# Performance work log

Measured on AMD Instinct MI355X. Metric: run time of the kernel, lower is better.

## Reference

```python
import jax, jax.numpy as jnp
import numpy as np

M, K, N = 32, 8192, 8192      # tokens, infeatures, outfeatures
GROUP = 128                   # quantization group size along K
PACK = 8                      # 32 bits / 4 bits per value


def _dequant(qweight, scales):
    """Unpack int4 nibbles (packed 8-per-int32 along K) and apply per-group
    symmetric dequant: w = (q - 8) * scale, matching Marlin's fused dequant."""
    kp, n = qweight.shape  # (K//8, N)
    shifts = (4 * jnp.arange(PACK, dtype=jnp.int32))[None, :, None]
    q = ((qweight[:, None, :] >> shifts) & 15)          # (K//8, 8, N)
    q = q.reshape(kp * PACK, n).astype(jnp.float32)     # (K, N)
    groups = scales.shape[0]
    gsz = (kp * PACK) // groups
    w = (q.reshape(groups, gsz, n) - 8.0) * scales[:, None, :]
    return w.reshape(kp * PACK, n)                      # (K, N) fp


def setup_inputs() -> dict:
    key = jax.random.key(0)
    kA, kQ, kS, kB = jax.random.split(key, 4)
    A = jax.random.normal(kA, (M, K), jnp.float32)
    # draw raw 4-bit codes then pack 8 of them into each int32 along K
    q4 = jax.random.randint(kQ, (K, N), 0, 16, jnp.int32)
    shifts = (4 * jnp.arange(PACK, dtype=jnp.int32))[None, :, None]
    qweight = jnp.sum(q4.reshape(K // PACK, PACK, N) << shifts, axis=1).astype(jnp.int32)
    scales = jax.random.uniform(kS, (K // GROUP, N), jnp.float32, 0.005, 0.02)
    bias = jax.random.normal(kB, (N,), jnp.float32) * 0.01
    return {"A": A, "qweight": qweight, "scales": scales, "bias": bias}


def reference(A, qweight, scales, bias):
    # Marlin mul(A, B, C, s) computes C = A @ dequant(B, s); then + bias
    W = _dequant(qweight, scales)          # (K, N)
    return A @ W + bias                    # (M, N)
```

## Files before the change

### kernel.cpp

```cpp
#include <hip/hip_runtime.h>
#include <hip/hip_bf16.h>
#include <stdint.h>

#define M_DIM 32
#define K_DIM 8192
#define N_DIM 8192
#define NGROUPS 64
#define KSPLIT 8
#define KPART (K_DIM / KSPLIT)
#define GPART (NGROUPS / KSPLIT)
#define BN 64

#define QSTRIDE 72
#define ASTRIDE 66

typedef __attribute__((ext_vector_type(8))) short short8;
typedef __attribute__((ext_vector_type(4))) float floatx4;

__global__ void marlin_prep_kernel(const float* __restrict__ A,
                                   uint16_t* __restrict__ Abf,
                                   float* __restrict__ R,
                                   float4* __restrict__ out4) {
    const int m = blockIdx.x;
    const int qtr = blockIdx.y;
    const int t = threadIdx.x;
    const int octet = qtr * 256 + t;
    const int k0 = octet * 8;

    {
        const int gtid = (qtr * 32 + m) * 256 + t;
        const float4 z = make_float4(0.f, 0.f, 0.f, 0.f);
        out4[gtid * 2] = z;
        out4[gtid * 2 + 1] = z;
    }

    const float* a = A + m * K_DIM + k0;
    uint16_t b[8];
    float sum = 0.f;
#pragma unroll
    for (int j = 0; j < 8; j++) {
        union { __hip_bfloat16 h; uint16_t u; } cv;
        cv.h = __float2bfloat16(a[j]);
        b[j] = cv.u;
        sum += __bfloat162float(cv.h);
    }
    uint32_t w0 = (uint32_t)b[0] | ((uint32_t)b[4] << 16);
    uint32_t w1 = (uint32_t)b[1] | ((uint32_t)b[5] << 16);
    uint32_t w2 = (uint32_t)b[2] | ((uint32_t)b[6] << 16);
    uint32_t w3 = (uint32_t)b[3] | ((uint32_t)b[7] << 16);
    *(uint4*)(Abf + (size_t)m * K_DIM + k0) = make_uint4(w0, w1, w2, w3);

#pragma unroll
    for (int off = 1; off < 16; off <<= 1) sum += __shfl_xor(sum, off, 16);
    if ((t & 15) == 0) R[m * NGROUPS + qtr * 16 + (t >> 4)] = sum;
}

__global__ __launch_bounds__(512, 4) void
MarlinQuantLinear_68556267979256_kernel(const int* __restrict__ qw,
                                        const float* __restrict__ scales,
                                        const float* __restrict__ bias,
                                        const uint16_t* __restrict__ Abf,
                                        const float* __restrict__ R,
                                        float* __restrict__ out) {
    __shared__ uint32_t qbuf[2][16 * QSTRIDE];
    __shared__ uint32_t abuf[2][32 * ASTRIDE];
    __shared__ float    r_lds[32 * 9];

    const int bx = blockIdx.x;
    const int bz = blockIdx.y;
    const int nbase = bx * BN;
    const int gbase = bz * GPART;

    const int tid = threadIdx.x;
    const int w = tid >> 6;
    const int lane = tid & 63;
    const int quad = lane >> 4;
    const int l16 = lane & 15;
    const int mtile = w & 1;
    const int ntile = w >> 1;
    const int ncol = nbase + ntile * 16 + l16;

    if (tid < 256) {
        const int mm = tid >> 3, gg = tid & 7;
        r_lds[mm * 9 + gg] = 136.0f * R[mm * NGROUPS + gbase + gg];
    }

    const float* scol = scales + (size_t)gbase * N_DIM + ncol;
    float s[GPART];
#pragma unroll
    for (int g = 0; g < GPART; g++) s[g] = scol[g * N_DIM];

    const int qr = tid >> 5;
    const int qc = (tid & 31) * 2;
    const int* qsrc = qw + ((size_t)(bz * 128 + qr) * N_DIM) + nbase + qc;
    const int am = tid >> 4;
    const int aseg = (tid & 15) * 4;
    const uint32_t* Ad = (const uint32_t*)Abf;
    const uint32_t* asrc = Ad + (size_t)am * (K_DIM / 2) + bz * (KPART / 2) + aseg;

    uint2 qst = *(const uint2*)(qsrc);
    uint4 ast = *(const uint4*)(asrc);

    floatx4 C = {0.f, 0.f, 0.f, 0.f};

#pragma unroll
    for (int g = 0; g < GPART; g++) {
        uint2 qnx; uint4 anx;
        if (g + 1 < GPART) {
            qnx = *(const uint2*)(qsrc + (size_t)(g + 1) * 16 * N_DIM);
            anx = *(const uint4*)(asrc + (g + 1) * 64);
        }
        *(uint2*)&qbuf[g & 1][qr * QSTRIDE + qc] = qst;
        *(uint4*)&abuf[g & 1][am * ASTRIDE + aseg] = ast;
        __syncthreads();

        floatx4 accg = {0.f, 0.f, 0.f, 0.f};
#pragma unroll
        for (int t = 0; t < 4; t++) {
            const uint32_t q = qbuf[g & 1][(t * 4 + quad) * QSTRIDE + ntile * 16 + l16];
            union { uint32_t u[4]; short8 v; } fb;
            fb.u[0] = ( q        & 0x000F000Fu) | 0x43004300u;
            fb.u[1] = ((q >> 4)  & 0x000F000Fu) | 0x43004300u;
            fb.u[2] = ((q >> 8)  & 0x000F000Fu) | 0x43004300u;
            fb.u[3] = ((q >> 12) & 0x000F000Fu) | 0x43004300u;
            const short8 fa =
                *(const short8*)&abuf[g & 1][(mtile * 16 + l16) * ASTRIDE + t * 16 + quad * 4];
            accg = __builtin_amdgcn_mfma_f32_16x16x32_bf16(fa, fb.v, accg, 0, 0, 0);
        }
#pragma unroll
        for (int r = 0; r < 4; r++) {
            const float tval = accg[r] - r_lds[(mtile * 16 + quad * 4 + r) * 9 + g];
            C[r] = fmaf(s[g], tval, C[r]);
        }
        qst = qnx;
        ast = anx;
    }

    const float bv = (bz == 0) ? bias[ncol] : 0.0f;
#pragma unroll
    for (int r = 0; r < 4; r++) {
        const int m = mtile * 16 + quad * 4 + r;
        atomicAdd(&out[(size_t)m * N_DIM + ncol], C[r] + bv);
    }
}

extern "C" void kernel_launch(void* const* d_in, const int* in_sizes, int n_in,
                              void* d_out, int out_size, void* d_ws, size_t ws_size,
                              hipStream_t stream) {
    const float* A      = (const float*)d_in[0];
    const int*   qw     = (const int*)d_in[1];
    const float* scales = (const float*)d_in[2];
    const float* bias   = (const float*)d_in[3];
    float* out = (float*)d_out;

    uint16_t* Abf = (uint16_t*)d_ws;
    float*    R   = (float*)((char*)d_ws + (size_t)M_DIM * K_DIM * 2);

    marlin_prep_kernel<<<dim3(M_DIM, 4), 256, 0, stream>>>(A, Abf, R, (float4*)out);
    MarlinQuantLinear_68556267979256_kernel<<<dim3(N_DIM / BN, KSPLIT), 512, 0, stream>>>(
        qw, scales, bias, Abf, R, out);
}
```

Measured before the change: 91.33 us.

## Replace atomic split-K accumulation with partial buffers and separate reduce kernel

The main kernel now writes per-split partial results to a workspace buffer instead of atomically adding into a zero-initialised output, and a new reduce kernel sums the eight partials and adds the bias. Each pipeline phase now stages two quantisation groups at once with wider 16-byte loads, which halves the number of barriers. The prep kernel no longer zeroes the output. This removes atomic contention and the zeroing pass, but adds a third launch plus roughly 8 MB of extra partial-buffer traffic.

```diff
diff --git a/kernel.cpp b/kernel.cpp
--- a/kernel.cpp
+++ b/kernel.cpp
@@ -10,29 +10,22 @@
 #define KPART (K_DIM / KSPLIT)
 #define GPART (NGROUPS / KSPLIT)
 #define BN 64
+#define NPH 4
 
 #define QSTRIDE 72
-#define ASTRIDE 66
+#define ASTRIDE 132
 
 typedef __attribute__((ext_vector_type(8))) short short8;
 typedef __attribute__((ext_vector_type(4))) float floatx4;
 
 __global__ void marlin_prep_kernel(const float* __restrict__ A,
                                    uint16_t* __restrict__ Abf,
-                                   float* __restrict__ R,
-                                   float4* __restrict__ out4) {
+                                   float* __restrict__ R) {
     const int m = blockIdx.x;
     const int qtr = blockIdx.y;
     const int t = threadIdx.x;
     const int octet = qtr * 256 + t;
     const int k0 = octet * 8;
-
-    {
-        const int gtid = (qtr * 32 + m) * 256 + t;
-        const float4 z = make_float4(0.f, 0.f, 0.f, 0.f);
-        out4[gtid * 2] = z;
-        out4[gtid * 2 + 1] = z;
-    }
 
     const float* a = A + m * K_DIM + k0;
     uint16_t b[8];
@@ -58,11 +51,10 @@
 __global__ __launch_bounds__(512, 4) void
 MarlinQuantLinear_68556267979256_kernel(const int* __restrict__ qw,
                                         const float* __restrict__ scales,
-                                        const float* __restrict__ bias,
                                         const uint16_t* __restrict__ Abf,
                                         const float* __restrict__ R,
-                                        float* __restrict__ out) {
-    __shared__ uint32_t qbuf[2][16 * QSTRIDE];
+                                        float* __restrict__ parts) {
+    __shared__ uint32_t qbuf[2][32 * QSTRIDE];
     __shared__ uint32_t abuf[2][32 * ASTRIDE];
     __shared__ float    r_lds[32 * 9];
 
@@ -80,68 +72,87 @@
     const int ntile = w >> 1;
     const int ncol = nbase + ntile * 16 + l16;
 
-    if (tid < 256) {
-        const int mm = tid >> 3, gg = tid & 7;
-        r_lds[mm * 9 + gg] = 136.0f * R[mm * NGROUPS + gbase + gg];
-    }
+    const int sr = tid >> 4;
+    const int sc = (tid & 15) * 4;
+    const int ac = (tid & 15) * 8;
+    const int* qsrc = qw + (size_t)(bz * 128 + sr) * N_DIM + nbase + sc;
+    const uint32_t* asrc = (const uint32_t*)Abf + (size_t)sr * (K_DIM / 2)
+                           + bz * (KPART / 2) + ac;
+
+    uint4 qst = *(const uint4*)qsrc;
+    uint4 a0  = *(const uint4*)asrc;
+    uint4 a1  = *(const uint4*)(asrc + 4);
 
     const float* scol = scales + (size_t)gbase * N_DIM + ncol;
     float s[GPART];
 #pragma unroll
     for (int g = 0; g < GPART; g++) s[g] = scol[g * N_DIM];
 
-    const int qr = tid >> 5;
-    const int qc = (tid & 31) * 2;
-    const int* qsrc = qw + ((size_t)(bz * 128 + qr) * N_DIM) + nbase + qc;
-    const int am = tid >> 4;
-    const int aseg = (tid & 15) * 4;
-    const uint32_t* Ad = (const uint32_t*)Abf;
-    const uint32_t* asrc = Ad + (size_t)am * (K_DIM / 2) + bz * (KPART / 2) + aseg;
-
-    uint2 qst = *(const uint2*)(qsrc);
-    uint4 ast = *(const uint4*)(asrc);
+    if (tid < 256) {
+        const int mm = tid >> 3, gg = tid & 7;
+        r_lds[mm * 9 + gg] = 136.0f * R[mm * NGROUPS + gbase + gg];
+    }
 
     floatx4 C = {0.f, 0.f, 0.f, 0.f};
 
 #pragma unroll
-    for (int g = 0; g < GPART; g++) {
-        uint2 qnx; uint4 anx;
-        if (g + 1 < GPART) {
-            qnx = *(const uint2*)(qsrc + (size_t)(g + 1) * 16 * N_DIM);
-            anx = *(const uint4*)(asrc + (g + 1) * 64);
+    for (int p = 0; p < NPH; p++) {
+        *(uint4*)&qbuf[p & 1][sr * QSTRIDE + sc] = qst;
+        *(uint4*)&abuf[p & 1][sr * ASTRIDE + ac] = a0;
+        *(uint4*)&abuf[p & 1][sr * ASTRIDE + ac + 4] = a1;
+        asm volatile("s_waitcnt lgkmcnt(0)" ::: "memory");
+        __builtin_amdgcn_s_barrier();
+
+        if (p + 1 < NPH) {
+            qst = *(const uint4*)(qsrc + (size_t)(p + 1) * 32 * N_DIM);
+            a0  = *(const uint4*)(asrc + (p + 1) * 128);
+            a1  = *(const uint4*)(asrc + (p + 1) * 128 + 4);
         }
-        *(uint2*)&qbuf[g & 1][qr * QSTRIDE + qc] = qst;
-        *(uint4*)&abuf[g & 1][am * ASTRIDE + aseg] = ast;
-        __syncthreads();
 
-        floatx4 accg = {0.f, 0.f, 0.f, 0.f};
 #pragma unroll
-        for (int t = 0; t < 4; t++) {
-            const uint32_t q = qbuf[g & 1][(t * 4 + quad) * QSTRIDE + ntile * 16 + l16];
-            union { uint32_t u[4]; short8 v; } fb;
-            fb.u[0] = ( q        & 0x000F000Fu) | 0x43004300u;
-            fb.u[1] = ((q >> 4)  & 0x000F000Fu) | 0x43004300u;
-            fb.u[2] = ((q >> 8)  & 0x000F000Fu) | 0x43004300u;
-            fb.u[3] = ((q >> 12) & 0x000F000Fu) | 0x43004300u;
-            const short8 fa =
-                *(const short8*)&abuf[g & 1][(mtile * 16 + l16) * ASTRIDE + t * 16 + quad * 4];
-            accg = __builtin_amdgcn_mfma_f32_16x16x32_bf16(fa, fb.v, accg, 0, 0, 0);
+        for (int gg = 0; gg < 2; gg++) {
+            floatx4 accg = {0.f, 0.f, 0.f, 0.f};
+#pragma unroll
+            for (int t = 0; t < 4; t++) {
+                const uint32_t q =
+                    qbuf[p & 1][(gg * 16 + t * 4 + quad) * QSTRIDE + ntile * 16 + l16];
+                union { uint32_t u[4]; short8 v; } fb;
+                fb.u[0] = ( q        & 0x000F000Fu) | 0x43004300u;
+                fb.u[1] = ((q >> 4)  & 0x000F000Fu) | 0x43004300u;
+                fb.u[2] = ((q >> 8)  & 0x000F000Fu) | 0x43004300u;
+                fb.u[3] = ((q >> 12) & 0x000F000Fu) | 0x43004300u;
+                const short8 fa = *(const short8*)
+                    &abuf[p & 1][(mtile * 16 + l16) * ASTRIDE + gg * 64 + t * 16 + quad * 4];
+                accg = __builtin_amdgcn_mfma_f32_16x16x32_bf16(fa, fb.v, accg, 0, 0, 0);
+            }
+            const int g = p * 2 + gg;
+#pragma unroll
+            for (int r = 0; r < 4; r++) {
+                const float tval = accg[r] - r_lds[(mtile * 16 + quad * 4 + r) * 9 + g];
+                C[r] = fmaf(s[g], tval, C[r]);
+            }
         }
-#pragma unroll
-        for (int r = 0; r < 4; r++) {
-            const float tval = accg[r] - r_lds[(mtile * 16 + quad * 4 + r) * 9 + g];
-            C[r] = fmaf(s[g], tval, C[r]);
-        }
-        qst = qnx;
-        ast = anx;
     }
 
-    const float bv = (bz == 0) ? bias[ncol] : 0.0f;
+    float* pp = parts + ((size_t)bz * M_DIM + mtile * 16 + quad * 4) * N_DIM + ncol;
 #pragma unroll
-    for (int r = 0; r < 4; r++) {
-        const int m = mtile * 16 + quad * 4 + r;
-        atomicAdd(&out[(size_t)m * N_DIM + ncol], C[r] + bv);
+    for (int r = 0; r < 4; r++) pp[r * N_DIM] = C[r];
+}
+
+__global__ __launch_bounds__(256) void
+marlin_reduce_kernel(const float* __restrict__ parts,
+                     const float* __restrict__ bias,
+                     float* __restrict__ out) {
+    const int idx = blockIdx.x * 256 + threadIdx.x;
+    const int c4 = idx & (N_DIM / 4 - 1);
+    const float4* p4 = (const float4*)parts;
+    float4 acc = *(const float4*)(bias + c4 * 4);
+#pragma unroll
+    for (int bz = 0; bz < KSPLIT; bz++) {
+        const float4 v = p4[(size_t)bz * (M_DIM * N_DIM / 4) + idx];
+        acc.x += v.x; acc.y += v.y; acc.z += v.z; acc.w += v.w;
     }
+    ((float4*)out)[idx] = acc;
 }
 
 extern "C" void kernel_launch(void* const* d_in, const int* in_sizes, int n_in,
@@ -153,10 +164,13 @@
     const float* bias   = (const float*)d_in[3];
     float* out = (float*)d_out;
 
-    uint16_t* Abf = (uint16_t*)d_ws;
-    float*    R   = (float*)((char*)d_ws + (size_t)M_DIM * K_DIM * 2);
+    uint16_t* Abf   = (uint16_t*)d_ws;
+    float*    R     = (float*)((char*)d_ws + (size_t)M_DIM * K_DIM * 2);
+    float*    parts = (float*)((char*)d_ws + (1 << 20));
 
-    marlin_prep_kernel<<<dim3(M_DIM, 4), 256, 0, stream>>>(A, Abf, R, (float4*)out);
+    marlin_prep_kernel<<<dim3(M_DIM, 4), 256, 0, stream>>>(A, Abf, R);
     MarlinQuantLinear_68556267979256_kernel<<<dim3(N_DIM / BN, KSPLIT), 512, 0, stream>>>(
-        qw, scales, bias, Abf, R, out);
+        qw, scales, Abf, R, parts);
+    marlin_reduce_kernel<<<dim3((M_DIM * N_DIM / 4) / 256), 256, 0, stream>>>(
+        parts, bias, out);
 }
```

New measurement: 93.96 us. 1.03x slower.

## Fuse A conversion into GEMM and drop split-K atomics for full-K blocks

Applied to the files above, without the earlier changes.

Removes the separate prep kernel: each block now reads fp32 A directly, converts it to bf16 and computes the per-group row sums in-register while staging to LDS. The split-K grid with atomicAdd output is replaced by one block per 32-column tile covering all of K, with two waves splitting each phase's K halves and reducing through LDS before a plain store. This removes a kernel launch, the workspace round trip and the output zeroing plus atomics. In exchange every block redundantly converts all of A, and the grid shrinks to 256 blocks with a long serial K loop.

```diff
diff --git a/kernel.cpp b/kernel.cpp
--- a/kernel.cpp
+++ b/kernel.cpp
@@ -6,141 +6,138 @@
 #define K_DIM 8192
 #define N_DIM 8192
 #define NGROUPS 64
-#define KSPLIT 8
-#define KPART (K_DIM / KSPLIT)
-#define GPART (NGROUPS / KSPLIT)
-#define BN 64
+#define BN 32
+#define NPH 32
 
-#define QSTRIDE 72
-#define ASTRIDE 66
+#define QS  33
+#define AST 132
+#define SST 36
 
 typedef __attribute__((ext_vector_type(8))) short short8;
 typedef __attribute__((ext_vector_type(4))) float floatx4;
 
-__global__ void marlin_prep_kernel(const float* __restrict__ A,
-                                   uint16_t* __restrict__ Abf,
-                                   float* __restrict__ R,
-                                   float4* __restrict__ out4) {
-    const int m = blockIdx.x;
-    const int qtr = blockIdx.y;
-    const int t = threadIdx.x;
-    const int octet = qtr * 256 + t;
-    const int k0 = octet * 8;
-
-    {
-        const int gtid = (qtr * 32 + m) * 256 + t;
-        const float4 z = make_float4(0.f, 0.f, 0.f, 0.f);
-        out4[gtid * 2] = z;
-        out4[gtid * 2 + 1] = z;
-    }
-
-    const float* a = A + m * K_DIM + k0;
-    uint16_t b[8];
-    float sum = 0.f;
-#pragma unroll
-    for (int j = 0; j < 8; j++) {
-        union { __hip_bfloat16 h; uint16_t u; } cv;
-        cv.h = __float2bfloat16(a[j]);
-        b[j] = cv.u;
-        sum += __bfloat162float(cv.h);
-    }
-    uint32_t w0 = (uint32_t)b[0] | ((uint32_t)b[4] << 16);
-    uint32_t w1 = (uint32_t)b[1] | ((uint32_t)b[5] << 16);
-    uint32_t w2 = (uint32_t)b[2] | ((uint32_t)b[6] << 16);
-    uint32_t w3 = (uint32_t)b[3] | ((uint32_t)b[7] << 16);
-    *(uint4*)(Abf + (size_t)m * K_DIM + k0) = make_uint4(w0, w1, w2, w3);
-
-#pragma unroll
-    for (int off = 1; off < 16; off <<= 1) sum += __shfl_xor(sum, off, 16);
-    if ((t & 15) == 0) R[m * NGROUPS + qtr * 16 + (t >> 4)] = sum;
-}
-
-__global__ __launch_bounds__(512, 4) void
-MarlinQuantLinear_68556267979256_kernel(const int* __restrict__ qw,
+__global__ __launch_bounds__(512, 2) void
+MarlinQuantLinear_68556267979256_kernel(const float* __restrict__ A,
+                                        const int* __restrict__ qw,
                                         const float* __restrict__ scales,
                                         const float* __restrict__ bias,
-                                        const uint16_t* __restrict__ Abf,
-                                        const float* __restrict__ R,
                                         float* __restrict__ out) {
-    __shared__ uint32_t qbuf[2][16 * QSTRIDE];
-    __shared__ uint32_t abuf[2][32 * ASTRIDE];
-    __shared__ float    r_lds[32 * 9];
+    __shared__ uint32_t qbuf[2][32 * QS];
+    __shared__ uint32_t abuf[2][32 * AST];
+    __shared__ float    s_lds[NGROUPS * SST];
+    __shared__ float    r_lds[32 * NGROUPS];
 
-    const int bx = blockIdx.x;
-    const int bz = blockIdx.y;
-    const int nbase = bx * BN;
-    const int gbase = bz * GPART;
-
+    const int nbase = blockIdx.x * BN;
     const int tid = threadIdx.x;
     const int w = tid >> 6;
     const int lane = tid & 63;
     const int quad = lane >> 4;
     const int l16 = lane & 15;
-    const int mtile = w & 1;
-    const int ntile = w >> 1;
-    const int ncol = nbase + ntile * 16 + l16;
+    const int kh = w >> 2;
+    const int mt = (w >> 1) & 1;
+    const int nt = w & 1;
 
-    if (tid < 256) {
-        const int mm = tid >> 3, gg = tid & 7;
-        r_lds[mm * 9 + gg] = 136.0f * R[mm * NGROUPS + gbase + gg];
+    const int qr = tid >> 4;
+    const int qc = (tid & 15) * 2;
+    const int ar = tid >> 4;
+    const int seg = tid & 15;
+
+    {
+        const int g = tid >> 3, c = (tid & 7) * 4;
+        *(float4*)&s_lds[g * SST + c] =
+            *(const float4*)(scales + (size_t)g * N_DIM + nbase + c);
     }
+    const float bv = bias[nbase + nt * 16 + l16];
 
-    const float* scol = scales + (size_t)gbase * N_DIM + ncol;
-    float s[GPART];
-#pragma unroll
-    for (int g = 0; g < GPART; g++) s[g] = scol[g * N_DIM];
-
-    const int qr = tid >> 5;
-    const int qc = (tid & 31) * 2;
-    const int* qsrc = qw + ((size_t)(bz * 128 + qr) * N_DIM) + nbase + qc;
-    const int am = tid >> 4;
-    const int aseg = (tid & 15) * 4;
-    const uint32_t* Ad = (const uint32_t*)Abf;
-    const uint32_t* asrc = Ad + (size_t)am * (K_DIM / 2) + bz * (KPART / 2) + aseg;
-
-    uint2 qst = *(const uint2*)(qsrc);
-    uint4 ast = *(const uint4*)(asrc);
-
+    float4 sa0[4], sa1[4];
+    uint2  sq0, sq1;
     floatx4 C = {0.f, 0.f, 0.f, 0.f};
 
+    auto ISSUE = [&](int p, float4 (&sa)[4], uint2& sq) {
+        sq = *(const uint2*)(qw + (size_t)(p * 32 + qr) * N_DIM + nbase + qc);
+        const float* ap = A + (size_t)ar * K_DIM + p * 256 + seg * 16;
 #pragma unroll
-    for (int g = 0; g < GPART; g++) {
-        uint2 qnx; uint4 anx;
-        if (g + 1 < GPART) {
-            qnx = *(const uint2*)(qsrc + (size_t)(g + 1) * 16 * N_DIM);
-            anx = *(const uint4*)(asrc + (g + 1) * 64);
+        for (int j = 0; j < 4; j++) sa[j] = *(const float4*)(ap + j * 4);
+    };
+
+    auto PHASE = [&](int p, float4 (&sa)[4], uint2& sq, bool doiss) {
+        uint32_t pk[8];
+        float rs = 0.f;
+#pragma unroll
+        for (int o = 0; o < 2; o++) {
+            union { float4 v[2]; float f[8]; } u;
+            u.v[0] = sa[2 * o];
+            u.v[1] = sa[2 * o + 1];
+            uint16_t b[8];
+#pragma unroll
+            for (int j = 0; j < 8; j++) {
+                union { __hip_bfloat16 h; uint16_t us; } cv;
+                cv.h = __float2bfloat16(u.f[j]);
+                b[j] = cv.us;
+                rs += __bfloat162float(cv.h);
+            }
+#pragma unroll
+            for (int j = 0; j < 4; j++)
+                pk[o * 4 + j] = (uint32_t)b[j] | ((uint32_t)b[j + 4] << 16);
         }
-        *(uint2*)&qbuf[g & 1][qr * QSTRIDE + qc] = qst;
-        *(uint4*)&abuf[g & 1][am * ASTRIDE + aseg] = ast;
-        __syncthreads();
+        rs += __shfl_xor(rs, 1);
+        rs += __shfl_xor(rs, 2);
+        rs += __shfl_xor(rs, 4);
+        if ((tid & 7) == 0)
+            r_lds[ar * NGROUPS + 2 * p + ((tid >> 3) & 1)] = 136.0f * rs;
 
-        floatx4 accg = {0.f, 0.f, 0.f, 0.f};
+        *(uint2*)&qbuf[p & 1][qr * QS + qc] = sq;
+        *(uint4*)&abuf[p & 1][ar * AST + seg * 8] = *(uint4*)&pk[0];
+        *(uint4*)&abuf[p & 1][ar * AST + seg * 8 + 4] = *(uint4*)&pk[4];
+        asm volatile("s_waitcnt lgkmcnt(0)" ::: "memory");
+        __builtin_amdgcn_s_barrier();
+
+        if (doiss) ISSUE(p + 2, sa, sq);
+
+        const uint32_t* qb = qbuf[p & 1];
+        const uint32_t* ab = abuf[p & 1];
+        floatx4 acc = {0.f, 0.f, 0.f, 0.f};
 #pragma unroll
         for (int t = 0; t < 4; t++) {
-            const uint32_t q = qbuf[g & 1][(t * 4 + quad) * QSTRIDE + ntile * 16 + l16];
+            const short8 fa = *(const short8*)
+                &ab[(mt * 16 + l16) * AST + kh * 64 + t * 16 + quad * 4];
+            const uint32_t q = qb[(kh * 16 + t * 4 + quad) * QS + nt * 16 + l16];
             union { uint32_t u[4]; short8 v; } fb;
             fb.u[0] = ( q        & 0x000F000Fu) | 0x43004300u;
             fb.u[1] = ((q >> 4)  & 0x000F000Fu) | 0x43004300u;
             fb.u[2] = ((q >> 8)  & 0x000F000Fu) | 0x43004300u;
             fb.u[3] = ((q >> 12) & 0x000F000Fu) | 0x43004300u;
-            const short8 fa =
-                *(const short8*)&abuf[g & 1][(mtile * 16 + l16) * ASTRIDE + t * 16 + quad * 4];
-            accg = __builtin_amdgcn_mfma_f32_16x16x32_bf16(fa, fb.v, accg, 0, 0, 0);
+            acc = __builtin_amdgcn_mfma_f32_16x16x32_bf16(fa, fb.v, acc, 0, 0, 0);
         }
+        const int g = 2 * p + kh;
+        const float sv = s_lds[g * SST + nt * 16 + l16];
 #pragma unroll
-        for (int r = 0; r < 4; r++) {
-            const float tval = accg[r] - r_lds[(mtile * 16 + quad * 4 + r) * 9 + g];
-            C[r] = fmaf(s[g], tval, C[r]);
-        }
-        qst = qnx;
-        ast = anx;
+        for (int r = 0; r < 4; r++)
+            C[r] = fmaf(sv, acc[r] - r_lds[(mt * 16 + quad * 4 + r) * NGROUPS + g], C[r]);
+    };
+
+    ISSUE(0, sa0, sq0);
+    ISSUE(1, sa1, sq1);
+#pragma unroll 1
+    for (int pp = 0; pp < NPH / 2; pp++) {
+        PHASE(2 * pp,     sa0, sq0, pp < NPH / 2 - 1);
+        PHASE(2 * pp + 1, sa1, sq1, pp < NPH / 2 - 1);
     }
 
-    const float bv = (bz == 0) ? bias[ncol] : 0.0f;
+    __syncthreads();
+    float* ex = (float*)abuf;
+    const int tile = mt * 2 + nt;
+    if (kh == 1) {
 #pragma unroll
-    for (int r = 0; r < 4; r++) {
-        const int m = mtile * 16 + quad * 4 + r;
-        atomicAdd(&out[(size_t)m * N_DIM + ncol], C[r] + bv);
+        for (int r = 0; r < 4; r++)
+            ex[tile * 256 + (quad * 4 + r) * 16 + l16] = C[r];
+    }
+    __syncthreads();
+    if (kh == 0) {
+#pragma unroll
+        for (int r = 0; r < 4; r++)
+            out[(size_t)(mt * 16 + quad * 4 + r) * N_DIM + nbase + nt * 16 + l16] =
+                C[r] + ex[tile * 256 + (quad * 4 + r) * 16 + l16] + bv;
     }
 }
 
@@ -152,11 +149,8 @@
     const float* scales = (const float*)d_in[2];
     const float* bias   = (const float*)d_in[3];
     float* out = (float*)d_out;
+    (void)d_ws; (void)ws_size;
 
-    uint16_t* Abf = (uint16_t*)d_ws;
-    float*    R   = (float*)((char*)d_ws + (size_t)M_DIM * K_DIM * 2);
-
-    marlin_prep_kernel<<<dim3(M_DIM, 4), 256, 0, stream>>>(A, Abf, R, (float4*)out);
-    MarlinQuantLinear_68556267979256_kernel<<<dim3(N_DIM / BN, KSPLIT), 512, 0, stream>>>(
-        qw, scales, bias, Abf, R, out);
+    MarlinQuantLinear_68556267979256_kernel<<<dim3(N_DIM / BN), 512, 0, stream>>>(
+        A, qw, scales, bias, out);
 }
```

After: 107.5 us. +17.7%, slower.
